# Kernel tuning notes

Measured on AMD Instinct MI355X. Metric: run time of the kernel, lower is better.

The kernel has to match this reference:

```python
import jax, jax.numpy as jnp
import numpy as np

VOCAB, INPUT, HIDDEN = 50000, 512, 1024
BATCH, MAX_LEN = 64, 256


def setup_inputs() -> dict:
    key = jax.random.key(0)
    ks = jax.random.split(key, 16)
    s = 0.02
    return {
        "last_output": jax.random.randint(ks[0], (BATCH,), 0, VOCAB),
        "last_hidden": jax.random.normal(ks[1], (BATCH, HIDDEN), jnp.float32),
        "encoder_outputs": jax.random.normal(ks[2], (MAX_LEN, BATCH, HIDDEN), jnp.float32),
        # embedding table (padding_idx=0 just means row 0 is a pad row; math is a plain gather)
        "embedding": jax.random.uniform(ks[3], (VOCAB, INPUT), jnp.float32, -0.25, 0.25),
        # concat attention: Linear(2H -> H) and v [H]
        "attn_W": jax.random.normal(ks[4], (HIDDEN, 2 * HIDDEN), jnp.float32) * s,
        "attn_b": jnp.zeros((HIDDEN,), jnp.float32),
        "v": jax.random.normal(ks[5], (HIDDEN,), jnp.float32) * s,
        # GRU (single layer): input size = INPUT + HIDDEN, gate order r,z,n (torch order)
        "W_ih": jax.random.normal(ks[6], (3 * HIDDEN, INPUT + HIDDEN), jnp.float32) * s,
        "W_hh": jax.random.uniform(ks[7], (3 * HIDDEN, HIDDEN), jnp.float32, -0.01, 0.01),
        "b_ih": jnp.zeros((3 * HIDDEN,), jnp.float32),
        "b_hh": jnp.zeros((3 * HIDDEN,), jnp.float32),
        # output projection Linear(2H -> vocab)
        "out_W": jax.random.normal(ks[8], (VOCAB, 2 * HIDDEN), jnp.float32) * s,
        "out_b": jnp.zeros((VOCAB,), jnp.float32),
    }


def reference(last_output, last_hidden, encoder_outputs, embedding,
              attn_W, attn_b, v, W_ih, W_hh, b_ih, b_hh, out_W, out_b):
    T, B, H = encoder_outputs.shape
    # --- embedding lookup: [B, INPUT]
    emb = embedding[last_output]

    # --- concat (Bahdanau-style, no tanh in original) attention, vectorized over T
    hid = jnp.broadcast_to(last_hidden[None], (T, B, H))
    cat = jnp.concatenate([hid, encoder_outputs], axis=-1)          # [T,B,2H]
    energy = jnp.einsum('tbk,hk->tbh', cat, attn_W) + attn_b        # [T,B,H]
    scores = jnp.einsum('tbh,h->bt', energy, v)                     # [B,T]
    attn = jax.nn.softmax(scores, axis=1)                           # [B,T]

    # --- context: [B,H]
    context = jnp.einsum('bt,tbh->bh', attn, encoder_outputs)

    # --- single GRU step (torch gate order r,z,n)
    x = jnp.concatenate([emb, context], axis=-1)                    # [B, INPUT+H]
    gi = x @ W_ih.T + b_ih                                          # [B,3H]
    gh = last_hidden @ W_hh.T + b_hh                                # [B,3H]
    i_r, i_z, i_n = jnp.split(gi, 3, axis=-1)
    h_r, h_z, h_n = jnp.split(gh, 3, axis=-1)
    r = jax.nn.sigmoid(i_r + h_r)
    z = jax.nn.sigmoid(i_z + h_z)
    n = jnp.tanh(i_n + r * h_n)
    h_new = (1.0 - z) * n + z * last_hidden                         # [B,H]

    # --- output projection + log_softmax over vocab
    logits = jnp.concatenate([h_new, context], axis=-1) @ out_W.T + out_b
    logp = jax.nn.log_softmax(logits, axis=-1)                      # [B,VOCAB]
    return logp, h_new
```

## Files before the change

### kernel.cpp

```cpp
#include <hip/hip_runtime.h>
#include <cstddef>

#define VOCAB  50000
#define INPUT  512
#define HIDDEN 1024
#define BATCH  64
#define MAXLEN 256
#define NTILE  3125

typedef float  f32x4 __attribute__((ext_vector_type(4)));
typedef __bf16 bf16x8 __attribute__((ext_vector_type(8)));

__device__ __forceinline__ bf16x8 cvt8(float4 a, float4 b) {
    bf16x8 r;
    r[0] = (__bf16)a.x; r[1] = (__bf16)a.y; r[2] = (__bf16)a.z; r[3] = (__bf16)a.w;
    r[4] = (__bf16)b.x; r[5] = (__bf16)b.y; r[6] = (__bf16)b.z; r[7] = (__bf16)b.w;
    return r;
}

__global__ void k_u2(const float* __restrict__ attn_W, const float* __restrict__ v,
                     float* __restrict__ u2) {
    int tid = threadIdx.x;
    int kk = blockIdx.x * 64 + (tid & 63);
    int hg = tid >> 6;
    float acc = 0.f;
#pragma unroll 8
    for (int h = hg * 256; h < hg * 256 + 256; ++h)
        acc += v[h] * attn_W[(size_t)h * (2 * HIDDEN) + HIDDEN + kk];
    __shared__ float red[4][64];
    red[hg][tid & 63] = acc;
    __syncthreads();
    if (tid < 64)
        u2[blockIdx.x * 64 + tid] = red[0][tid] + red[1][tid] + red[2][tid] + red[3][tid];
}

__global__ void k_scores_pack(const float* __restrict__ enc, const float* __restrict__ u2,
                              float* __restrict__ scores,
                              const int* __restrict__ last_output,
                              const float* __restrict__ embedding,
                              const float* __restrict__ hid,
                              __bf16* __restrict__ x_bf, __bf16* __restrict__ hid_bf) {
    int bid = blockIdx.x, tid = threadIdx.x;
    if (bid < 4096) {
        int wid = tid >> 6, lane = tid & 63;
        int p = bid * 4 + wid;
        const float* row = enc + (size_t)p * HIDDEN;
        float acc = 0.f;
#pragma unroll
        for (int i = 0; i < 4; ++i) {
            float4 e = *(const float4*)(row + lane * 4 + i * 256);
            float4 u = *(const float4*)(u2  + lane * 4 + i * 256);
            acc += e.x * u.x + e.y * u.y + e.z * u.z + e.w * u.w;
        }
#pragma unroll
        for (int off = 32; off; off >>= 1) acc += __shfl_down(acc, off, 64);
        if (lane == 0) scores[(p & 63) * MAXLEN + (p >> 6)] = acc;
    } else {
        int idx = (bid - 4096) * 256 + tid;
        if (idx < 64 * INPUT) {
            int b = idx >> 9, k = idx & 511;
            x_bf[b * 1536 + k] = (__bf16)embedding[(size_t)last_output[b] * INPUT + k];
        } else {
            idx -= 64 * INPUT;
            int b = idx >> 10, h = idx & 1023;
            hid_bf[b * HIDDEN + h] = (__bf16)hid[b * HIDDEN + h];
        }
    }
}

__global__ void k_ctx(const float* __restrict__ enc, const float* __restrict__ scores,
                      __bf16* __restrict__ x_bf, __bf16* __restrict__ y_bf) {
    int b = blockIdx.x >> 2, hc = blockIdx.x & 3, tid = threadIdx.x;
    __shared__ float a[256];
    __shared__ float red[256];
    float s = scores[b * MAXLEN + tid];
    red[tid] = s; __syncthreads();
    for (int off = 128; off; off >>= 1) { if (tid < off) red[tid] = fmaxf(red[tid], red[tid + off]); __syncthreads(); }
    float m = red[0]; __syncthreads();
    float e = expf(s - m);
    red[tid] = e; __syncthreads();
    for (int off = 128; off; off >>= 1) { if (tid < off) red[tid] += red[tid + off]; __syncthreads(); }
    a[tid] = e * (1.f / red[0]);
    __syncthreads();
    int h = hc * 256 + tid;
    float acc = 0.f;
#pragma unroll 8
    for (int t = 0; t < MAXLEN; ++t)
        acc += a[t] * enc[((size_t)(t * BATCH + b)) * HIDDEN + h];
    x_bf[b * 1536 + INPUT + h]   = (__bf16)acc;
    y_bf[b * 2048 + HIDDEN + h]  = (__bf16)acc;
}

__device__ __forceinline__ void gemm_tile(const float* __restrict__ W,
                                          const float* __restrict__ bias,
                                          const __bf16* __restrict__ A,
                                          float* __restrict__ out,
                                          int N, int K, int jt, int tid) {
    int wid = tid >> 6, lane = tid & 63;
    int j  = jt * 16 + (lane & 15);
    int kg = (lane >> 4) * 8;
    int kchunk = K >> 2;
    int kbeg = wid * kchunk, kend = kbeg + kchunk;
    const float*  wrow = W + (size_t)j * K;
    const __bf16* arow = A + (size_t)(lane & 15) * K;
    f32x4 acc[4] = {};
    for (int k0 = kbeg; k0 < kend; k0 += 32) {
        int kk = k0 + kg;
        float4 w0 = *(const float4*)(wrow + kk);
        float4 w1 = *(const float4*)(wrow + kk + 4);
        bf16x8 bw = cvt8(w0, w1);
#pragma unroll
        for (int mt = 0; mt < 4; ++mt) {
            bf16x8 av = *(const bf16x8*)(arow + (size_t)mt * 16 * K + kk);
            acc[mt] = __builtin_amdgcn_mfma_f32_16x16x32_bf16(av, bw, acc[mt], 0, 0, 0);
        }
    }
    __shared__ float lds[4][1024];
#pragma unroll
    for (int mt = 0; mt < 4; ++mt)
#pragma unroll
        for (int r = 0; r < 4; ++r) {
            int m = mt * 16 + (lane >> 4) * 4 + r;
            lds[wid][m * 16 + (lane & 15)] = acc[mt][r];
        }
    __syncthreads();
#pragma unroll
    for (int o = tid; o < 1024; o += 256) {
        float s = lds[0][o] + lds[1][o] + lds[2][o] + lds[3][o];
        int m = o >> 4, jl = o & 15;
        int jj = jt * 16 + jl;
        out[(size_t)m * N + jj] = s + bias[jj];
    }
}

__global__ __launch_bounds__(256) void k_gemm_gru(const float* __restrict__ W_ih,
                                                  const float* __restrict__ b_ih,
                                                  const __bf16* __restrict__ x_bf,
                                                  float* __restrict__ Gi,
                                                  const float* __restrict__ W_hh,
                                                  const float* __restrict__ b_hh,
                                                  const __bf16* __restrict__ hid_bf,
                                                  float* __restrict__ Gh) {
    int bid = blockIdx.x, tid = threadIdx.x;
    if (bid < 192) gemm_tile(W_ih, b_ih, x_bf,  Gi, 3072, 1536, bid,       tid);
    else           gemm_tile(W_hh, b_hh, hid_bf, Gh, 3072, 1024, bid - 192, tid);
}

__global__ void k_combine(const float* __restrict__ Gi, const float* __restrict__ Gh,
                          const float* __restrict__ hid, float* __restrict__ hnew_out,
                          __bf16* __restrict__ y_bf) {
    int idx = blockIdx.x * 256 + threadIdx.x;
    int b = idx >> 10, h = idx & 1023;
    const float* gi = Gi + (size_t)b * 3072;
    const float* gh = Gh + (size_t)b * 3072;
    float r  = 1.f / (1.f + expf(-(gi[h] + gh[h])));
    float z  = 1.f / (1.f + expf(-(gi[1024 + h] + gh[1024 + h])));
    float n  = tanhf(gi[2048 + h] + r * gh[2048 + h]);
    float hp = hid[b * HIDDEN + h];
    float hn = (1.f - z) * n + z * hp;
    hnew_out[b * HIDDEN + h] = hn;
    y_bf[b * 2048 + h] = (__bf16)hn;
}

__global__ __launch_bounds__(256) void k_gemv(const float* __restrict__ W,
                                              const float* __restrict__ bias,
                                              const __bf16* __restrict__ A,
                                              float* __restrict__ out,
                                              float* __restrict__ mw,
                                              float* __restrict__ sw) {
    int bid = blockIdx.x, tid = threadIdx.x;
    int wid = tid >> 6, lane = tid & 63;
    int kg = (lane >> 4) * 8;
    int kbeg = wid * 512, kend = kbeg + 512;
    int ntiles = (bid == 1562) ? 1 : 2;
    int j0 = bid * 32 + (lane & 15);
    int jr0 = min(j0,      VOCAB - 1);
    int jr1 = min(j0 + 16, VOCAB - 1);
    const float*  wrow0 = W + (size_t)jr0 * 2048;
    const float*  wrow1 = W + (size_t)jr1 * 2048;
    const __bf16* arow  = A + (size_t)(lane & 15) * 2048;
    f32x4 acc[2][4] = {};
    for (int k0 = kbeg; k0 < kend; k0 += 32) {
        int kk = k0 + kg;
        float4 p0 = *(const float4*)(wrow0 + kk);
        float4 p1 = *(const float4*)(wrow0 + kk + 4);
        float4 q0 = *(const float4*)(wrow1 + kk);
        float4 q1 = *(const float4*)(wrow1 + kk + 4);
        bf16x8 bw0 = cvt8(p0, p1);
        bf16x8 bw1 = cvt8(q0, q1);
#pragma unroll
        for (int mt = 0; mt < 4; ++mt) {
            bf16x8 av = *(const bf16x8*)(arow + (size_t)mt * 16 * 2048 + kk);
            acc[0][mt] = __builtin_amdgcn_mfma_f32_16x16x32_bf16(av, bw0, acc[0][mt], 0, 0, 0);
            acc[1][mt] = __builtin_amdgcn_mfma_f32_16x16x32_bf16(av, bw1, acc[1][mt], 0, 0, 0);
        }
    }
    __shared__ float lds[4][1024];
    for (int u = 0; u < ntiles; ++u) {
        if (u) __syncthreads();
#pragma unroll
        for (int mt = 0; mt < 4; ++mt)
#pragma unroll
            for (int r = 0; r < 4; ++r) {
                int m = mt * 16 + (lane >> 4) * 4 + r;
                lds[wid][m * 16 + (lane & 15)] = acc[u][mt][r];
            }
        __syncthreads();
#pragma unroll
        for (int o = tid; o < 1024; o += 256) {
            float s = lds[0][o] + lds[1][o] + lds[2][o] + lds[3][o];
            int m = o >> 4, jl = o & 15;
            int jj = bid * 32 + u * 16 + jl;
            s += bias[jj];
            out[(size_t)m * VOCAB + jj] = s;
            lds[0][o] = s;
        }
        __syncthreads();
        if (tid < 64) {
            int m = tid;
            float mx = -INFINITY;
#pragma unroll
            for (int jl = 0; jl < 16; ++jl) mx = fmaxf(mx, lds[0][m * 16 + jl]);
            float se = 0.f;
#pragma unroll
            for (int jl = 0; jl < 16; ++jl) se += expf(lds[0][m * 16 + jl] - mx);
            int tile = bid * 2 + u;
            mw[(size_t)m * NTILE + tile] = mx;
            sw[(size_t)m * NTILE + tile] = se;
        }
    }
}

__global__ void k_lse_combine(const float* __restrict__ mw, const float* __restrict__ sw,
                              float* __restrict__ lse) {
    int b = blockIdx.x, tid = threadIdx.x;
    __shared__ float red[256];
    const float* mrow = mw + (size_t)b * NTILE;
    const float* srow = sw + (size_t)b * NTILE;
    float m = -INFINITY;
    for (int i = tid; i < NTILE; i += 256) m = fmaxf(m, mrow[i]);
    red[tid] = m; __syncthreads();
    for (int off = 128; off; off >>= 1) { if (tid < off) red[tid] = fmaxf(red[tid], red[tid + off]); __syncthreads(); }
    m = red[0]; __syncthreads();
    float s = 0.f;
    for (int i = tid; i < NTILE; i += 256) s += srow[i] * expf(mrow[i] - m);
    red[tid] = s; __syncthreads();
    for (int off = 128; off; off >>= 1) { if (tid < off) red[tid] += red[tid + off]; __syncthreads(); }
    if (tid == 0) lse[b] = m + logf(red[0]);
}

__global__ void k_lse_sub(float* __restrict__ logits, const float* __restrict__ lse) {
    int idx = blockIdx.x * 256 + threadIdx.x;
    size_t f = (size_t)idx * 4;
    float l = lse[(int)(f / VOCAB)];
    float4 x = *(float4*)(logits + f);
    x.x -= l; x.y -= l; x.z -= l; x.w -= l;
    *(float4*)(logits + f) = x;
}

extern "C" void kernel_launch(void* const* d_in, const int* in_sizes, int n_in,
                              void* d_out, int out_size, void* d_ws, size_t ws_size,
                              hipStream_t stream) {
    const int*   last_output = (const int*)  d_in[0];
    const float* last_hidden = (const float*)d_in[1];
    const float* enc         = (const float*)d_in[2];
    const float* embedding   = (const float*)d_in[3];
    const float* attn_W      = (const float*)d_in[4];
    const float* v           = (const float*)d_in[6];
    const float* W_ih        = (const float*)d_in[7];
    const float* W_hh        = (const float*)d_in[8];
    const float* b_ih        = (const float*)d_in[9];
    const float* b_hh        = (const float*)d_in[10];
    const float* out_W       = (const float*)d_in[11];
    const float* out_b       = (const float*)d_in[12];

    float* out_logp = (float*)d_out;
    float* out_hnew = (float*)d_out + (size_t)BATCH * VOCAB;

    char* ws = (char*)d_ws;
    float*  u2      = (float*) (ws + 0);
    float*  scores  = (float*) (ws + 4096);
    __bf16* x_bf    = (__bf16*)(ws + 69632);
    __bf16* hid_bf  = (__bf16*)(ws + 266240);
    __bf16* y_bf    = (__bf16*)(ws + 397312);
    float*  Gi      = (float*) (ws + 659456);
    float*  Gh      = (float*) (ws + 1445888);
    float*  mw      = (float*) (ws + 2232320);
    float*  sw      = (float*) (ws + 3032320);
    float*  lse     = (float*) (ws + 3832320);

    k_u2          <<<16,   256, 0, stream>>>(attn_W, v, u2);
    k_scores_pack <<<4480, 256, 0, stream>>>(enc, u2, scores, last_output, embedding,
                                             last_hidden, x_bf, hid_bf);
    k_ctx         <<<256,  256, 0, stream>>>(enc, scores, x_bf, y_bf);
    k_gemm_gru    <<<384,  256, 0, stream>>>(W_ih, b_ih, x_bf, Gi, W_hh, b_hh, hid_bf, Gh);
    k_combine     <<<256,  256, 0, stream>>>(Gi, Gh, last_hidden, out_hnew, y_bf);
    k_gemv        <<<1563, 256, 0, stream>>>(out_W, out_b, y_bf, out_logp, mw, sw);
    k_lse_combine <<<64,   256, 0, stream>>>(mw, sw, lse);
    k_lse_sub     <<<3125, 256, 0, stream>>>(out_logp, lse);
}
```

Baseline: 220.8 us.

## Fuse pre-GEMV stages and LSE stages into cooperative kernels with grid syncs

Merges the u2, scores, context, GRU GEMM and GRU combine stages into one cooperative kernel of 256 blocks separated by grid.sync, and fuses the LSE combine and subtract into a second cooperative kernel. The GEMV now merges its two tiles' max/sum in registers, which halves the partial LSE entries. This removes launch gaps and tail effects between many small kernels. In exchange, each phase is limited to 256 blocks, which may reduce parallelism in the scores and GEMM phases, and grid syncs add their own cost.

```diff
diff --git a/kernel.cpp b/kernel.cpp
--- a/kernel.cpp
+++ b/kernel.cpp
@@ -1,12 +1,15 @@
 #include <hip/hip_runtime.h>
+#include <hip/hip_cooperative_groups.h>
 #include <cstddef>
+
+namespace cg = cooperative_groups;
 
 #define VOCAB  50000
 #define INPUT  512
 #define HIDDEN 1024
 #define BATCH  64
 #define MAXLEN 256
-#define NTILE  3125
+#define NBLK   1563
 
 typedef float  f32x4 __attribute__((ext_vector_type(4)));
 typedef __bf16 bf16x8 __attribute__((ext_vector_type(8)));
@@ -18,84 +21,12 @@
     return r;
 }
 
-__global__ void k_u2(const float* __restrict__ attn_W, const float* __restrict__ v,
-                     float* __restrict__ u2) {
-    int tid = threadIdx.x;
-    int kk = blockIdx.x * 64 + (tid & 63);
-    int hg = tid >> 6;
-    float acc = 0.f;
-#pragma unroll 8
-    for (int h = hg * 256; h < hg * 256 + 256; ++h)
-        acc += v[h] * attn_W[(size_t)h * (2 * HIDDEN) + HIDDEN + kk];
-    __shared__ float red[4][64];
-    red[hg][tid & 63] = acc;
-    __syncthreads();
-    if (tid < 64)
-        u2[blockIdx.x * 64 + tid] = red[0][tid] + red[1][tid] + red[2][tid] + red[3][tid];
-}
-
-__global__ void k_scores_pack(const float* __restrict__ enc, const float* __restrict__ u2,
-                              float* __restrict__ scores,
-                              const int* __restrict__ last_output,
-                              const float* __restrict__ embedding,
-                              const float* __restrict__ hid,
-                              __bf16* __restrict__ x_bf, __bf16* __restrict__ hid_bf) {
-    int bid = blockIdx.x, tid = threadIdx.x;
-    if (bid < 4096) {
-        int wid = tid >> 6, lane = tid & 63;
-        int p = bid * 4 + wid;
-        const float* row = enc + (size_t)p * HIDDEN;
-        float acc = 0.f;
-#pragma unroll
-        for (int i = 0; i < 4; ++i) {
-            float4 e = *(const float4*)(row + lane * 4 + i * 256);
-            float4 u = *(const float4*)(u2  + lane * 4 + i * 256);
-            acc += e.x * u.x + e.y * u.y + e.z * u.z + e.w * u.w;
-        }
-#pragma unroll
-        for (int off = 32; off; off >>= 1) acc += __shfl_down(acc, off, 64);
-        if (lane == 0) scores[(p & 63) * MAXLEN + (p >> 6)] = acc;
-    } else {
-        int idx = (bid - 4096) * 256 + tid;
-        if (idx < 64 * INPUT) {
-            int b = idx >> 9, k = idx & 511;
-            x_bf[b * 1536 + k] = (__bf16)embedding[(size_t)last_output[b] * INPUT + k];
-        } else {
-            idx -= 64 * INPUT;
-            int b = idx >> 10, h = idx & 1023;
-            hid_bf[b * HIDDEN + h] = (__bf16)hid[b * HIDDEN + h];
-        }
-    }
-}
-
-__global__ void k_ctx(const float* __restrict__ enc, const float* __restrict__ scores,
-                      __bf16* __restrict__ x_bf, __bf16* __restrict__ y_bf) {
-    int b = blockIdx.x >> 2, hc = blockIdx.x & 3, tid = threadIdx.x;
-    __shared__ float a[256];
-    __shared__ float red[256];
-    float s = scores[b * MAXLEN + tid];
-    red[tid] = s; __syncthreads();
-    for (int off = 128; off; off >>= 1) { if (tid < off) red[tid] = fmaxf(red[tid], red[tid + off]); __syncthreads(); }
-    float m = red[0]; __syncthreads();
-    float e = expf(s - m);
-    red[tid] = e; __syncthreads();
-    for (int off = 128; off; off >>= 1) { if (tid < off) red[tid] += red[tid + off]; __syncthreads(); }
-    a[tid] = e * (1.f / red[0]);
-    __syncthreads();
-    int h = hc * 256 + tid;
-    float acc = 0.f;
-#pragma unroll 8
-    for (int t = 0; t < MAXLEN; ++t)
-        acc += a[t] * enc[((size_t)(t * BATCH + b)) * HIDDEN + h];
-    x_bf[b * 1536 + INPUT + h]   = (__bf16)acc;
-    y_bf[b * 2048 + HIDDEN + h]  = (__bf16)acc;
-}
-
 __device__ __forceinline__ void gemm_tile(const float* __restrict__ W,
                                           const float* __restrict__ bias,
                                           const __bf16* __restrict__ A,
                                           float* __restrict__ out,
-                                          int N, int K, int jt, int tid) {
+                                          int N, int K, int jt, int tid,
+                                          float (*lds)[1024]) {
     int wid = tid >> 6, lane = tid & 63;
     int j  = jt * 16 + (lane & 15);
     int kg = (lane >> 4) * 8;
@@ -115,7 +46,7 @@
             acc[mt] = __builtin_amdgcn_mfma_f32_16x16x32_bf16(av, bw, acc[mt], 0, 0, 0);
         }
     }
-    __shared__ float lds[4][1024];
+    __syncthreads();
 #pragma unroll
     for (int mt = 0; mt < 4; ++mt)
 #pragma unroll
@@ -128,38 +59,116 @@
     for (int o = tid; o < 1024; o += 256) {
         float s = lds[0][o] + lds[1][o] + lds[2][o] + lds[3][o];
         int m = o >> 4, jl = o & 15;
-        int jj = jt * 16 + jl;
-        out[(size_t)m * N + jj] = s + bias[jj];
-    }
-}
-
-__global__ __launch_bounds__(256) void k_gemm_gru(const float* __restrict__ W_ih,
-                                                  const float* __restrict__ b_ih,
-                                                  const __bf16* __restrict__ x_bf,
-                                                  float* __restrict__ Gi,
-                                                  const float* __restrict__ W_hh,
-                                                  const float* __restrict__ b_hh,
-                                                  const __bf16* __restrict__ hid_bf,
-                                                  float* __restrict__ Gh) {
+        out[(size_t)m * N + jt * 16 + jl] = s + bias[jt * 16 + jl];
+    }
+}
+
+__global__ __launch_bounds__(256) void k_pre(
+    const float* __restrict__ attn_W, const float* __restrict__ v,
+    const float* __restrict__ enc,
+    const int* __restrict__ last_output, const float* __restrict__ embedding,
+    const float* __restrict__ hid,
+    float* __restrict__ u2p, float* __restrict__ scores,
+    __bf16* __restrict__ x_bf, __bf16* __restrict__ hid_bf, __bf16* __restrict__ y_bf,
+    const float* __restrict__ W_ih, const float* __restrict__ b_ih, float* __restrict__ Gi,
+    const float* __restrict__ W_hh, const float* __restrict__ b_hh, float* __restrict__ Gh,
+    float* __restrict__ out_hnew)
+{
+    cg::grid_group grid = cg::this_grid();
     int bid = blockIdx.x, tid = threadIdx.x;
-    if (bid < 192) gemm_tile(W_ih, b_ih, x_bf,  Gi, 3072, 1536, bid,       tid);
-    else           gemm_tile(W_hh, b_hh, hid_bf, Gh, 3072, 1024, bid - 192, tid);
-}
-
-__global__ void k_combine(const float* __restrict__ Gi, const float* __restrict__ Gh,
-                          const float* __restrict__ hid, float* __restrict__ hnew_out,
-                          __bf16* __restrict__ y_bf) {
-    int idx = blockIdx.x * 256 + threadIdx.x;
-    int b = idx >> 10, h = idx & 1023;
-    const float* gi = Gi + (size_t)b * 3072;
-    const float* gh = Gh + (size_t)b * 3072;
-    float r  = 1.f / (1.f + expf(-(gi[h] + gh[h])));
-    float z  = 1.f / (1.f + expf(-(gi[1024 + h] + gh[1024 + h])));
-    float n  = tanhf(gi[2048 + h] + r * gh[2048 + h]);
-    float hp = hid[b * HIDDEN + h];
-    float hn = (1.f - z) * n + z * hp;
-    hnew_out[b * HIDDEN + h] = hn;
-    y_bf[b * 2048 + h] = (__bf16)hn;
+    __shared__ float lds4[4][1024];
+    __shared__ float a_s[256];
+    __shared__ float red[256];
+    __shared__ float u2s[1024];
+
+    {
+        int kc = bid & 63, hq = bid >> 6;
+        int k = kc * 16 + (tid & 15);
+        int h0 = hq * 256 + (tid >> 4) * 16;
+        float acc = 0.f;
+#pragma unroll
+        for (int i = 0; i < 16; ++i) {
+            int h = h0 + i;
+            acc += v[h] * attn_W[(size_t)h * (2 * HIDDEN) + HIDDEN + k];
+        }
+        lds4[0][tid] = acc;
+        __syncthreads();
+        if (tid < 16) {
+            float s = 0.f;
+#pragma unroll
+            for (int hg = 0; hg < 16; ++hg) s += lds4[0][hg * 16 + tid];
+            u2p[hq * 1024 + kc * 16 + tid] = s;
+        }
+    }
+    __threadfence(); grid.sync();
+
+    for (int i = tid; i < 1024; i += 256)
+        u2s[i] = u2p[i] + u2p[1024 + i] + u2p[2048 + i] + u2p[3072 + i];
+    __syncthreads();
+    {
+        int wid = tid >> 6, lane = tid & 63;
+        int wg = bid * 4 + wid;
+#pragma unroll 2
+        for (int r = 0; r < 16; ++r) {
+            int p = wg * 16 + r;
+            const float* row = enc + (size_t)p * HIDDEN;
+            float acc = 0.f;
+#pragma unroll
+            for (int i = 0; i < 4; ++i) {
+                float4 e = *(const float4*)(row + lane * 4 + i * 256);
+                float4 u = *(const float4*)(&u2s[lane * 4 + i * 256]);
+                acc += e.x * u.x + e.y * u.y + e.z * u.z + e.w * u.w;
+            }
+#pragma unroll
+            for (int off = 32; off; off >>= 1) acc += __shfl_down(acc, off, 64);
+            if (lane == 0) scores[(p & 63) * MAXLEN + (p >> 6)] = acc;
+        }
+    }
+    __threadfence(); grid.sync();
+
+    {
+        int b = bid >> 2, hc = bid & 3;
+        float s = scores[b * MAXLEN + tid];
+        red[tid] = s; __syncthreads();
+        for (int off = 128; off; off >>= 1) { if (tid < off) red[tid] = fmaxf(red[tid], red[tid + off]); __syncthreads(); }
+        float m = red[0]; __syncthreads();
+        float e = expf(s - m);
+        red[tid] = e; __syncthreads();
+        for (int off = 128; off; off >>= 1) { if (tid < off) red[tid] += red[tid + off]; __syncthreads(); }
+        a_s[tid] = e * (1.f / red[0]);
+        __syncthreads();
+        int h = hc * 256 + tid;
+        float acc = 0.f;
+#pragma unroll 8
+        for (int t = 0; t < MAXLEN; ++t)
+            acc += a_s[t] * enc[(size_t)(t * BATCH + b) * HIDDEN + h];
+        x_bf[b * 1536 + INPUT + h]  = (__bf16)acc;
+        y_bf[b * 2048 + HIDDEN + h] = (__bf16)acc;
+        if (tid < 128)
+            x_bf[b * 1536 + hc * 128 + tid] =
+                (__bf16)embedding[(size_t)last_output[b] * INPUT + hc * 128 + tid];
+        hid_bf[b * HIDDEN + hc * 256 + tid] = (__bf16)hid[b * HIDDEN + hc * 256 + tid];
+    }
+    __threadfence(); grid.sync();
+
+    if (bid < 192) gemm_tile(W_ih, b_ih, x_bf,   Gi, 3072, 1536, bid,       tid, lds4);
+    else           gemm_tile(W_hh, b_hh, hid_bf, Gh, 3072, 1024, bid - 192, tid, lds4);
+    if (bid < 128) gemm_tile(W_hh, b_hh, hid_bf, Gh, 3072, 1024, bid + 64,  tid, lds4);
+    __threadfence(); grid.sync();
+
+    {
+        int idx = bid * 256 + tid;
+        int b = idx >> 10, h = idx & 1023;
+        const float* gi = Gi + (size_t)b * 3072;
+        const float* gh = Gh + (size_t)b * 3072;
+        float r  = 1.f / (1.f + expf(-(gi[h] + gh[h])));
+        float z  = 1.f / (1.f + expf(-(gi[1024 + h] + gh[1024 + h])));
+        float n  = tanhf(gi[2048 + h] + r * gh[2048 + h]);
+        float hp = hid[b * HIDDEN + h];
+        float hn = (1.f - z) * n + z * hp;
+        out_hnew[b * HIDDEN + h] = hn;
+        y_bf[b * 2048 + h] = (__bf16)hn;
+    }
 }
 
 __global__ __launch_bounds__(256) void k_gemv(const float* __restrict__ W,
@@ -172,7 +181,7 @@
     int wid = tid >> 6, lane = tid & 63;
     int kg = (lane >> 4) * 8;
     int kbeg = wid * 512, kend = kbeg + 512;
-    int ntiles = (bid == 1562) ? 1 : 2;
+    int ntiles = (bid == NBLK - 1) ? 1 : 2;
     int j0 = bid * 32 + (lane & 15);
     int jr0 = min(j0,      VOCAB - 1);
     int jr1 = min(j0 + 16, VOCAB - 1);
@@ -196,6 +205,7 @@
         }
     }
     __shared__ float lds[4][1024];
+    float Mreg = -INFINITY, Sreg = 0.f;
     for (int u = 0; u < ntiles; ++u) {
         if (u) __syncthreads();
 #pragma unroll
@@ -217,45 +227,52 @@
         }
         __syncthreads();
         if (tid < 64) {
-            int m = tid;
             float mx = -INFINITY;
 #pragma unroll
-            for (int jl = 0; jl < 16; ++jl) mx = fmaxf(mx, lds[0][m * 16 + jl]);
+            for (int jl = 0; jl < 16; ++jl) mx = fmaxf(mx, lds[0][tid * 16 + jl]);
             float se = 0.f;
 #pragma unroll
-            for (int jl = 0; jl < 16; ++jl) se += expf(lds[0][m * 16 + jl] - mx);
-            int tile = bid * 2 + u;
-            mw[(size_t)m * NTILE + tile] = mx;
-            sw[(size_t)m * NTILE + tile] = se;
-        }
-    }
-}
-
-__global__ void k_lse_combine(const float* __restrict__ mw, const float* __restrict__ sw,
-                              float* __restrict__ lse) {
-    int b = blockIdx.x, tid = threadIdx.x;
+            for (int jl = 0; jl < 16; ++jl) se += expf(lds[0][tid * 16 + jl] - mx);
+            float M2 = fmaxf(Mreg, mx);
+            Sreg = Sreg * expf(Mreg - M2) + se * expf(mx - M2);
+            Mreg = M2;
+        }
+    }
+    if (tid < 64) {
+        mw[(size_t)tid * NBLK + bid] = Mreg;
+        sw[(size_t)tid * NBLK + bid] = Sreg;
+    }
+}
+
+__global__ __launch_bounds__(256) void k_post(float* __restrict__ logits,
+                                              const float* __restrict__ mw,
+                                              const float* __restrict__ sw,
+                                              float* __restrict__ lse) {
+    cg::grid_group grid = cg::this_grid();
+    int bid = blockIdx.x, tid = threadIdx.x;
     __shared__ float red[256];
-    const float* mrow = mw + (size_t)b * NTILE;
-    const float* srow = sw + (size_t)b * NTILE;
-    float m = -INFINITY;
-    for (int i = tid; i < NTILE; i += 256) m = fmaxf(m, mrow[i]);
-    red[tid] = m; __syncthreads();
-    for (int off = 128; off; off >>= 1) { if (tid < off) red[tid] = fmaxf(red[tid], red[tid + off]); __syncthreads(); }
-    m = red[0]; __syncthreads();
-    float s = 0.f;
-    for (int i = tid; i < NTILE; i += 256) s += srow[i] * expf(mrow[i] - m);
-    red[tid] = s; __syncthreads();
-    for (int off = 128; off; off >>= 1) { if (tid < off) red[tid] += red[tid + off]; __syncthreads(); }
-    if (tid == 0) lse[b] = m + logf(red[0]);
-}
-
-__global__ void k_lse_sub(float* __restrict__ logits, const float* __restrict__ lse) {
-    int idx = blockIdx.x * 256 + threadIdx.x;
-    size_t f = (size_t)idx * 4;
-    float l = lse[(int)(f / VOCAB)];
-    float4 x = *(float4*)(logits + f);
-    x.x -= l; x.y -= l; x.z -= l; x.w -= l;
-    *(float4*)(logits + f) = x;
+    if (bid < 64) {
+        const float* mrow = mw + (size_t)bid * NBLK;
+        const float* srow = sw + (size_t)bid * NBLK;
+        float m = -INFINITY;
+        for (int i = tid; i < NBLK; i += 256) m = fmaxf(m, mrow[i]);
+        red[tid] = m; __syncthreads();
+        for (int off = 128; off; off >>= 1) { if (tid < off) red[tid] = fmaxf(red[tid], red[tid + off]); __syncthreads(); }
+        m = red[0]; __syncthreads();
+        float s = 0.f;
+        for (int i = tid; i < NBLK; i += 256) s += srow[i] * expf(mrow[i] - m);
+        red[tid] = s; __syncthreads();
+        for (int off = 128; off; off >>= 1) { if (tid < off) red[tid] += red[tid + off]; __syncthreads(); }
+        if (tid == 0) lse[bid] = m + logf(red[0]);
+    }
+    __threadfence(); grid.sync();
+    for (int idx = bid * 256 + tid; idx < (BATCH * VOCAB) / 4; idx += 256 * 256) {
+        size_t f = (size_t)idx * 4;
+        float l = lse[(int)(f / VOCAB)];
+        float4 x = *(float4*)(logits + f);
+        x.x -= l; x.y -= l; x.z -= l; x.w -= l;
+        *(float4*)(logits + f) = x;
+    }
 }
 
 extern "C" void kernel_launch(void* const* d_in, const int* in_sizes, int n_in,
@@ -278,24 +295,26 @@
     float* out_hnew = (float*)d_out + (size_t)BATCH * VOCAB;
 
     char* ws = (char*)d_ws;
-    float*  u2      = (float*) (ws + 0);
-    float*  scores  = (float*) (ws + 4096);
-    __bf16* x_bf    = (__bf16*)(ws + 69632);
-    __bf16* hid_bf  = (__bf16*)(ws + 266240);
-    __bf16* y_bf    = (__bf16*)(ws + 397312);
-    float*  Gi      = (float*) (ws + 659456);
-    float*  Gh      = (float*) (ws + 1445888);
-    float*  mw      = (float*) (ws + 2232320);
-    float*  sw      = (float*) (ws + 3032320);
-    float*  lse     = (float*) (ws + 3832320);
-
-    k_u2          <<<16,   256, 0, stream>>>(attn_W, v, u2);
-    k_scores_pack <<<4480, 256, 0, stream>>>(enc, u2, scores, last_output, embedding,
-                                             last_hidden, x_bf, hid_bf);
-    k_ctx         <<<256,  256, 0, stream>>>(enc, scores, x_bf, y_bf);
-    k_gemm_gru    <<<384,  256, 0, stream>>>(W_ih, b_ih, x_bf, Gi, W_hh, b_hh, hid_bf, Gh);
-    k_combine     <<<256,  256, 0, stream>>>(Gi, Gh, last_hidden, out_hnew, y_bf);
-    k_gemv        <<<1563, 256, 0, stream>>>(out_W, out_b, y_bf, out_logp, mw, sw);
-    k_lse_combine <<<64,   256, 0, stream>>>(mw, sw, lse);
-    k_lse_sub     <<<3125, 256, 0, stream>>>(out_logp, lse);
-}
+    float*  u2p     = (float*) (ws + 0);
+    float*  scores  = (float*) (ws + 16384);
+    __bf16* x_bf    = (__bf16*)(ws + 81920);
+    __bf16* hid_bf  = (__bf16*)(ws + 278528);
+    __bf16* y_bf    = (__bf16*)(ws + 409600);
+    float*  Gi      = (float*) (ws + 671744);
+    float*  Gh      = (float*) (ws + 1458176);
+    float*  mw      = (float*) (ws + 2244608);
+    float*  sw      = (float*) (ws + 2644736);
+    float*  lse     = (float*) (ws + 3044864);
+
+    void* a1[] = {(void*)&attn_W, (void*)&v, (void*)&enc, (void*)&last_output,
+                  (void*)&embedding, (void*)&last_hidden, (void*)&u2p, (void*)&scores,
+                  (void*)&x_bf, (void*)&hid_bf, (void*)&y_bf,
+                  (void*)&W_ih, (void*)&b_ih, (void*)&Gi,
+                  (void*)&W_hh, (void*)&b_hh, (void*)&Gh, (void*)&out_hnew};
+    hipLaunchCooperativeKernel((void*)k_pre, dim3(256), dim3(256), a1, 0, stream);
+
+    k_gemv<<<NBLK, 256, 0, stream>>>(out_W, out_b, y_bf, out_logp, mw, sw);
+
+    void* a2[] = {(void*)&out_logp, (void*)&mw, (void*)&sw, (void*)&lse};
+    hipLaunchCooperativeKernel((void*)k_post, dim3(256), dim3(256), a2, 0, stream);
+}
```

New measurement: 489.8 us. +121.8%, slower.
